# Performance work log

Hardware: AMD Instinct MI355X
Metric: run time of the kernel (lower is better)

## Reference

```python
import jax, jax.numpy as jnp
import numpy as np

B, C, E, H = 2, 2048, 1024, 16
HD = E // H


def setup_inputs() -> dict:
    key = jax.random.key(0)
    k_x, k_len, k_w1, k_b1, k_w2, k_b2 = jax.random.split(key, 6)
    x = jax.random.normal(k_x, (B, C, E), dtype=jnp.float32)
    # pad_mask: True where token is valid; random valid lengths in [C//2, C]
    lengths = jax.random.randint(k_len, (B,), C // 2, C + 1)
    pad_mask = jnp.arange(C)[None, :] < lengths[:, None]  # [B, C] bool
    s1 = 1.0 / np.sqrt(E)
    w_qkv = jax.random.uniform(k_w1, (3 * E, E), jnp.float32, -s1, s1)  # torch Linear weight [out,in]
    b_qkv = jax.random.uniform(k_b1, (3 * E,), jnp.float32, -s1, s1)
    w_out = jax.random.uniform(k_w2, (E, E), jnp.float32, -s1, s1)
    b_out = jax.random.uniform(k_b2, (E,), jnp.float32, -s1, s1)
    return {"x": x, "pad_mask": pad_mask, "w_qkv": w_qkv, "b_qkv": b_qkv,
            "w_out": w_out, "b_out": b_out}


def reference(x, pad_mask, w_qkv, b_qkv, w_out, b_out):
    b, c, e = x.shape
    qkv = x @ w_qkv.T + b_qkv                      # [B, C, 3E]
    qkv = qkv.reshape(b, c, 3, H, HD)
    qkv = jnp.transpose(qkv, (2, 0, 3, 1, 4))      # [3, B, H, C, HD]
    q, k, v = qkv[0], qkv[1], qkv[2]
    scores = jnp.einsum('bhqd,bhkd->bhqk', q, k) / np.sqrt(HD)  # [B,H,C,C]
    causal = jnp.tril(jnp.ones((c, c), dtype=bool))
    scores = jnp.where(causal[None, None, :, :], scores, -1e9)
    scores = jnp.where(pad_mask[:, None, None, :], scores, -1e9)
    attn = jax.nn.softmax(scores, axis=-1)
    out = jnp.einsum('bhqk,bhkd->bhqd', attn, v)   # [B,H,C,HD]
    out = jnp.transpose(out, (0, 2, 1, 3)).reshape(b, c, e)
    return out @ w_out.T + b_out
```

## Files before the change

### kernel.cpp

```cpp
#include <hip/hip_runtime.h>
#include <cstdint>
#include <cstddef>

typedef short short8 __attribute__((ext_vector_type(8)));
typedef float f32x4 __attribute__((ext_vector_type(4)));

#define NB 2
#define NC 2048
#define NE 1024
#define NH 16
#define ND 64
#define QSZ (NB*NH*NC*ND)

typedef const __attribute__((address_space(1))) void GV;
typedef __attribute__((address_space(3))) void LV;

__device__ __forceinline__ unsigned short f32_to_bf16(float f) {
    union { float f; unsigned u; } v; v.f = f;
    return (unsigned short)((v.u + 0x7fffu + ((v.u >> 16) & 1u)) >> 16);
}

__global__ __launch_bounds__(256) void fused_cast_kernel(
    const float* __restrict__ x, const float* __restrict__ wqkv,
    const float* __restrict__ wout, const void* __restrict__ pad,
    unsigned short* __restrict__ x_bf, unsigned short* __restrict__ wqkv_bf,
    unsigned short* __restrict__ wout_bf, int* __restrict__ lengths)
{
    const int bid = blockIdx.x, tid = threadIdx.x;
    if (bid < 8192) {
        const float* src; unsigned short* dst; int i;
        if (bid < 4096)      { src = x;    dst = x_bf;    i = bid*256 + tid; }
        else if (bid < 7168) { src = wqkv; dst = wqkv_bf; i = (bid-4096)*256 + tid; }
        else                 { src = wout; dst = wout_bf; i = (bid-7168)*256 + tid; }
        float4 v = ((const float4*)src)[i];
        ushort4 o;
        o.x = f32_to_bf16(v.x); o.y = f32_to_bf16(v.y);
        o.z = f32_to_bf16(v.z); o.w = f32_to_bf16(v.w);
        ((ushort4*)dst)[i] = o;
    } else {
        const int b = bid - 8192;
        unsigned w0 = ((const unsigned*)pad)[0];
        int cnt = 0;
        for (int i = tid; i < NC; i += 256) {
            int idx = b*NC + i;
            bool valid;
            if (w0 == 1u)               valid = ((const int*)pad)[idx] != 0;
            else if (w0 == 0x3f800000u) valid = ((const float*)pad)[idx] != 0.0f;
            else                        valid = ((const unsigned char*)pad)[idx] != 0;
            cnt += valid ? 1 : 0;
        }
        cnt += __shfl_xor(cnt, 1);  cnt += __shfl_xor(cnt, 2);
        cnt += __shfl_xor(cnt, 4);  cnt += __shfl_xor(cnt, 8);
        cnt += __shfl_xor(cnt, 16); cnt += __shfl_xor(cnt, 32);
        __shared__ int ws_[4];
        if ((tid & 63) == 0) ws_[tid >> 6] = cnt;
        __syncthreads();
        if (tid == 0) lengths[b] = ws_[0] + ws_[1] + ws_[2] + ws_[3];
    }
}

template<int EPI, int TM, int WPE>
__global__ __launch_bounds__(256, WPE) void gemm_bt_kernel(
    const unsigned short* __restrict__ A,
    const unsigned short* __restrict__ Bw,
    const float* __restrict__ bias,
    const int* __restrict__ lengths,
    float* __restrict__ outF,
    unsigned short* __restrict__ outQ,
    int M, int N, int K)
{
    constexpr int NF = (TM == 128) ? 4 : 2;
    constexpr int WCW = 16 * NF;
    __shared__ unsigned short As[TM*64];
    __shared__ unsigned short Bs[128*64];
    const int tid = threadIdx.x;
    const int w = tid >> 6, lane = tid & 63;
    const int wr = (TM == 128) ? (w >> 1) : 0;
    const int wc = (TM == 128) ? (w & 1) : w;
    const int g = lane >> 4, lr = lane & 15;
    const int nbx = N >> 7, nwg = gridDim.x;
    const int id = blockIdx.x;
    const int swz = (id & 7) * (nwg >> 3) + (id >> 3);
    const int mBase = (swz / nbx) * TM, nBase = (swz % nbx) * 128;

    if constexpr (EPI == 1) {
        if (nBase >= 1024) {
            const int lb = lengths[mBase >> 11];
            if ((mBase & 2047) >= ((lb + 63) & ~63)) return;
        }
    }

    f32x4 acc[4][NF];
#pragma unroll
    for (int m = 0; m < 4; ++m)
#pragma unroll
        for (int n = 0; n < NF; ++n) acc[m][n] = (f32x4){0.f, 0.f, 0.f, 0.f};

    constexpr int AJ = TM / 32;
    int srow[4], scol[4]; unsigned ldso[4];
#pragma unroll
    for (int j = 0; j < 4; ++j) {
        int o = ((j*4 + w) << 10) + lane*16;
        int row = o >> 7;
        int chunk = ((o >> 4) & 7) ^ (row & 7);
        srow[j] = row; scol[j] = chunk * 8; ldso[j] = (unsigned)((j*4 + w) << 10);
    }

    const int nk = K >> 6;
    for (int kt = 0; kt < nk; ++kt) {
        const int k0 = kt << 6;
#pragma unroll
        for (int j = 0; j < AJ; ++j) {
            const unsigned short* ga = A + (size_t)(mBase + srow[j])*K + (k0 + scol[j]);
            __builtin_amdgcn_global_load_lds((GV*)ga, (LV*)((char*)As + ldso[j]), 16, 0, 0);
        }
#pragma unroll
        for (int j = 0; j < 4; ++j) {
            const unsigned short* gb = Bw + (size_t)(nBase + srow[j])*K + (k0 + scol[j]);
            __builtin_amdgcn_global_load_lds((GV*)gb, (LV*)((char*)Bs + ldso[j]), 16, 0, 0);
        }
        __syncthreads();
#pragma unroll
        for (int ks = 0; ks < 2; ++ks) {
            short8 af[4], bf[NF];
#pragma unroll
            for (int m = 0; m < 4; ++m) {
                int row = wr*64 + m*16 + lr;
                int chunk = (ks*4 + g) ^ (row & 7);
                af[m] = *(const short8*)((const char*)As + row*128 + chunk*16);
            }
#pragma unroll
            for (int n = 0; n < NF; ++n) {
                int row = wc*WCW + n*16 + lr;
                int chunk = (ks*4 + g) ^ (row & 7);
                bf[n] = *(const short8*)((const char*)Bs + row*128 + chunk*16);
            }
#pragma unroll
            for (int m = 0; m < 4; ++m)
#pragma unroll
                for (int n = 0; n < NF; ++n)
                    acc[m][n] = __builtin_amdgcn_mfma_f32_16x16x32_bf16(af[m], bf[n], acc[m][n], 0, 0, 0);
        }
        __syncthreads();
    }

    if constexpr (EPI == 0) {
#pragma unroll
        for (int n = 0; n < NF; ++n) {
            int col = nBase + wc*WCW + n*16 + lr;
            float bv = bias[col];
#pragma unroll
            for (int m = 0; m < 4; ++m) {
                int rowb = mBase + wr*64 + m*16 + 4*g;
#pragma unroll
                for (int r = 0; r < 4; ++r)
                    outF[(size_t)(rowb + r)*N + col] = acc[m][n][r] + bv;
            }
        }
    } else {
        if (nBase >= 2048) {
#pragma unroll
            for (int n = 0; n < NF; ++n) {
                int col = nBase + wc*WCW + n*16 + lr;
                float bv = bias[col];
                int hh = (col >> 6) & 15, d = col & 63;
#pragma unroll
                for (int m = 0; m < 4; ++m) {
                    int rowb = mBase + wr*64 + m*16 + 4*g;
                    int bb = rowb >> 11, c = rowb & 2047;
                    int cp = (c & ~63) | ((m >> 1) << 5) | (g << 3) | ((m & 1) << 2);
                    size_t base = (((size_t)((4 + bb)*16 + hh))*64 + d)*2048 + cp;
                    float v0 = acc[m][n][0] + bv, v1 = acc[m][n][1] + bv;
                    float v2 = acc[m][n][2] + bv, v3 = acc[m][n][3] + bv;
                    unsigned w0, w1;
                    asm("v_cvt_pk_bf16_f32 %0, %1, %2" : "=v"(w0) : "v"(v0), "v"(v1));
                    asm("v_cvt_pk_bf16_f32 %0, %1, %2" : "=v"(w1) : "v"(v2), "v"(v3));
                    union { unsigned u[2]; uint2 v; } pk2; pk2.u[0] = w0; pk2.u[1] = w1;
                    *(uint2*)(outQ + base) = pk2.v;
                }
            }
        } else {
#pragma unroll
            for (int n = 0; n < NF; ++n) {
                int col = nBase + wc*WCW + n*16 + lr;
                float bv = bias[col];
                int t = col >> 10, hh = (col >> 6) & 15, d = col & 63;
                float qscale = (t == 0) ? 0.1803368801f : 1.0f;
#pragma unroll
                for (int m = 0; m < 4; ++m) {
                    int rowb = mBase + wr*64 + m*16 + 4*g;
#pragma unroll
                    for (int r = 0; r < 4; ++r) {
                        int row = rowb + r;
                        int bb = row >> 11, c = row & 2047;
                        unsigned short bf16v = f32_to_bf16((acc[m][n][r] + bv) * qscale);
                        size_t idx = ((((size_t)(t*2 + bb))*16 + hh)*2048 + c)*64 + d;
                        outQ[idx] = bf16v;
                    }
                }
            }
        }
    }
}

__global__ __launch_bounds__(256, 4) void attn_kernel(
    const unsigned short* __restrict__ qkv,
    const int* __restrict__ lengths,
    unsigned short* __restrict__ ctx)
{
    __shared__ unsigned short Kt[2][64*64];
    __shared__ unsigned short Vt[2][64*64];
    const int bh = blockIdx.x;
    const int b = bh >> 4, h = bh & 15;
    const int y = blockIdx.y;
    const int qb = (y < 8) ? 31 - y : (y < 16) ? y - 8 : (y < 24) ? 39 - y : y - 16;
    const int q0 = qb * 64;
    const int len = lengths[b];
    const int nt = min(qb + 1, (len + 63) >> 6);
    const int tid = threadIdx.x, w = tid >> 6, lane = tid & 63;
    const int g = lane >> 4, lr = lane & 15;
    const unsigned short* qp = qkv +          ((size_t)(b*NH + h))*NC*ND;
    const unsigned short* kp = qkv + QSZ    + ((size_t)(b*NH + h))*NC*ND;
    const unsigned short* vp = qkv + 2*QSZ  + ((size_t)(b*NH + h))*ND*NC;
    const int qw0 = q0 + w*16;

    short8 aq[2];
#pragma unroll
    for (int ks = 0; ks < 2; ++ks)
        aq[ks] = *(const short8*)(qp + (size_t)(qw0 + lr)*ND + ks*32 + 8*g);

    f32x4 oa[4];
#pragma unroll
    for (int n = 0; n < 4; ++n) oa[n] = (f32x4){0.f, 0.f, 0.f, 0.f};
    f32x4 acc_l = (f32x4){0.f, 0.f, 0.f, 0.f};
    union { unsigned u[4]; short8 s; } ones;
    ones.u[0] = ones.u[1] = ones.u[2] = ones.u[3] = 0x3F803F80u;

    int srw[2], sck[2]; unsigned ldso[2];
#pragma unroll
    for (int j = 0; j < 2; ++j) {
        int o = ((j*4 + w) << 10) + lane*16;
        int row = o >> 7;
        int chunk = ((o >> 4) & 7) ^ (row & 7);
        srw[j] = row; sck[j] = chunk * 8; ldso[j] = (unsigned)((j*4 + w) << 10);
    }

#define STAGE(T, BUF) do {                                                        \
    int k0s = (T) << 6;                                                           \
    _Pragma("unroll")                                                             \
    for (int j = 0; j < 2; ++j) {                                                 \
        const unsigned short* gk = kp + (size_t)(k0s + srw[j])*ND + sck[j];       \
        const unsigned short* gv = vp + (size_t)srw[j]*NC + k0s + sck[j];         \
        __builtin_amdgcn_global_load_lds((GV*)gk, (LV*)((char*)Kt[BUF] + ldso[j]), 16, 0, 0); \
        __builtin_amdgcn_global_load_lds((GV*)gv, (LV*)((char*)Vt[BUF] + ldso[j]), 16, 0, 0); \
    } } while (0)

    STAGE(0, 0);
    __syncthreads();

#pragma unroll 2
    for (int t = 0; t < nt; ++t) {
        if (t + 1 < nt) STAGE(t + 1, (t + 1) & 1);
        const char* Kb = (const char*)Kt[t & 1];
        const char* Vb = (const char*)Vt[t & 1];
        const int k0 = t << 6;

        f32x4 sa[4];
#pragma unroll
        for (int a = 0; a < 4; ++a) sa[a] = (f32x4){0.f, 0.f, 0.f, 0.f};
        __builtin_amdgcn_s_setprio(1);
#pragma unroll
        for (int ks = 0; ks < 2; ++ks) {
#pragma unroll
            for (int a = 0; a < 4; ++a) {
                int row = a*16 + lr;
                int chunk = (ks*4 + g) ^ (row & 7);
                short8 ak = *(const short8*)(Kb + row*128 + chunk*16);
                sa[a] = __builtin_amdgcn_mfma_f32_16x16x32_bf16(ak, aq[ks], sa[a], 0, 0, 0);
            }
        }
        __builtin_amdgcn_s_setprio(0);

        float p[4][4];
        const bool edge = (t == nt - 1);
        if (!edge) {
#pragma unroll
            for (int a = 0; a < 4; ++a)
#pragma unroll
                for (int r = 0; r < 4; ++r)
                    p[a][r] = exp2f(sa[a][r]);
        } else {
            const int qg = qw0 + lr;
            const int kb0 = k0 + 4*g;
#pragma unroll
            for (int a = 0; a < 4; ++a)
#pragma unroll
                for (int r = 0; r < 4; ++r) {
                    int key = kb0 + 16*a + r;
                    p[a][r] = (key <= qg && key < len) ? exp2f(sa[a][r]) : 0.f;
                }
        }

        unsigned pw0, pw1, pw2, pw3, pw4, pw5, pw6, pw7;
        asm("v_cvt_pk_bf16_f32 %0, %1, %2" : "=v"(pw0) : "v"(p[0][0]), "v"(p[0][1]));
        asm("v_cvt_pk_bf16_f32 %0, %1, %2" : "=v"(pw1) : "v"(p[0][2]), "v"(p[0][3]));
        asm("v_cvt_pk_bf16_f32 %0, %1, %2" : "=v"(pw2) : "v"(p[1][0]), "v"(p[1][1]));
        asm("v_cvt_pk_bf16_f32 %0, %1, %2" : "=v"(pw3) : "v"(p[1][2]), "v"(p[1][3]));
        asm("v_cvt_pk_bf16_f32 %0, %1, %2" : "=v"(pw4) : "v"(p[2][0]), "v"(p[2][1]));
        asm("v_cvt_pk_bf16_f32 %0, %1, %2" : "=v"(pw5) : "v"(p[2][2]), "v"(p[2][3]));
        asm("v_cvt_pk_bf16_f32 %0, %1, %2" : "=v"(pw6) : "v"(p[3][0]), "v"(p[3][1]));
        asm("v_cvt_pk_bf16_f32 %0, %1, %2" : "=v"(pw7) : "v"(p[3][2]), "v"(p[3][3]));
        union { unsigned u[4]; short8 s; } pu0, pu1;
        pu0.u[0] = pw0; pu0.u[1] = pw1; pu0.u[2] = pw2; pu0.u[3] = pw3;
        pu1.u[0] = pw4; pu1.u[1] = pw5; pu1.u[2] = pw6; pu1.u[3] = pw7;

        __builtin_amdgcn_s_setprio(1);
#pragma unroll
        for (int ks = 0; ks < 2; ++ks) {
            short8 pa = ks ? pu1.s : pu0.s;
            acc_l = __builtin_amdgcn_mfma_f32_16x16x32_bf16(pa, ones.s, acc_l, 0, 0, 0);
#pragma unroll
            for (int n = 0; n < 4; ++n) {
                int row = n*16 + lr;
                int chunk = (ks*4 + g) ^ (row & 7);
                short8 bv = *(const short8*)(Vb + row*128 + chunk*16);
                oa[n] = __builtin_amdgcn_mfma_f32_16x16x32_bf16(pa, bv, oa[n], 0, 0, 0);
            }
        }
        __builtin_amdgcn_s_setprio(0);

        __syncthreads();
    }
#undef STAGE

#pragma unroll
    for (int r = 0; r < 4; ++r) {
        float inv = 1.0f / acc_l[r];
        int qg = qw0 + 4*g + r;
        size_t base = ((size_t)b*NC + qg)*NE + h*ND;
#pragma unroll
        for (int n = 0; n < 4; ++n)
            ctx[base + n*16 + lr] = f32_to_bf16(oa[n][r] * inv);
    }
}

extern "C" void kernel_launch(void* const* d_in, const int* in_sizes, int n_in,
                              void* d_out, int out_size, void* d_ws, size_t ws_size,
                              hipStream_t stream)
{
    const float* x    = (const float*)d_in[0];
    const void*  pad  = d_in[1];
    const float* wqkv = (const float*)d_in[2];
    const float* bqkv = (const float*)d_in[3];
    const float* wout = (const float*)d_in[4];
    const float* bout = (const float*)d_in[5];
    float* out = (float*)d_out;

    unsigned short* x_bf    = (unsigned short*)d_ws;
    unsigned short* wqkv_bf = x_bf    + 4194304;
    unsigned short* wout_bf = wqkv_bf + 3145728;
    unsigned short* qkv     = wout_bf + 1048576;
    unsigned short* ctx     = qkv     + 12582912;
    int*            lens    = (int*)(ctx + 4194304);

    fused_cast_kernel<<<8194, 256, 0, stream>>>(x, wqkv, wout, pad,
                                                x_bf, wqkv_bf, wout_bf, lens);

    gemm_bt_kernel<1,128,3><<<768, 256, 0, stream>>>(x_bf, wqkv_bf, bqkv, lens,
                                                     nullptr, qkv, 4096, 3072, 1024);
    attn_kernel<<<dim3(32, 32), 256, 0, stream>>>(qkv, lens, ctx);
    gemm_bt_kernel<0,64,2><<<512, 256, 0, stream>>>(ctx, wout_bf, bout, nullptr,
                                                    out, nullptr, 4096, 1024, 1024);
}
```

Baseline: 90.90 us.

## Replace QKV GEMM with 256x256-tile, 8-wave pipelined kernel

Adds a dedicated QKV projection kernel that uses 256x256 output tiles with 512 threads, double-buffered direct-to-LDS loads with swizzling, and interleaved MFMA phases under s_setprio. The larger tiles raise arithmetic intensity, and the staged barrier schedule overlaps global loads with matrix math. It keeps the skip of K/V tiles past the padded length and writes the same Q/K/V/V-transposed layouts. The launch drops to 192 blocks, which may underfill the CUs on MI355X, and the high LDS and register use limits occupancy. The output GEMM now receives lens, which is probably unused in that epilogue.

```diff
diff --git a/kernel.cpp b/kernel.cpp
--- a/kernel.cpp
+++ b/kernel.cpp
@@ -59,6 +59,180 @@
     }
 }
 
+__global__ __launch_bounds__(512, 2) void gemm_qkv256_kernel(
+    const unsigned short* __restrict__ A,
+    const unsigned short* __restrict__ Bw,
+    const float* __restrict__ bias,
+    const int* __restrict__ lengths,
+    unsigned short* __restrict__ outQ)
+{
+    __shared__ unsigned short As[2*256*64];
+    __shared__ unsigned short Bs[2*256*64];
+    const int tid = threadIdx.x;
+    const int w = tid >> 6, lane = tid & 63;
+    const int wr = w >> 2, wc = w & 3;
+    const int g = lane >> 4, lr = lane & 15;
+    const int id = blockIdx.x;
+    const int swz = (id & 7) * 24 + (id >> 3);
+    const int mBase = (swz / 12) * 256, nBase = (swz % 12) * 256;
+
+    if (nBase >= 1024) {
+        const int lb = lengths[mBase >> 11];
+        if ((mBase & 2047) >= ((lb + 63) & ~63)) return;
+    }
+
+    f32x4 acc[8][4];
+#pragma unroll
+    for (int m = 0; m < 8; ++m)
+#pragma unroll
+        for (int n = 0; n < 4; ++n) acc[m][n] = (f32x4){0.f, 0.f, 0.f, 0.f};
+
+    const int srow = tid >> 3;
+    const int gcol = (((tid & 7) ^ ((tid >> 3) & 7)) << 3);
+    const unsigned ldw = (unsigned)(w << 10);
+
+#define STA(kt, h, buf) do { _Pragma("unroll")                                     \
+    for (int u = 0; u < 2; ++u) {                                                  \
+        const unsigned short* gp = A + (size_t)(mBase + (h)*128 + u*64 + srow)*1024 \
+                                     + ((kt) << 6) + gcol;                         \
+        __builtin_amdgcn_global_load_lds((GV*)gp,                                  \
+            (LV*)((char*)As + (buf)*32768 + (h)*16384 + u*8192 + ldw), 16, 0, 0);  \
+    } } while (0)
+#define STB(kt, h, buf) do { _Pragma("unroll")                                     \
+    for (int u = 0; u < 2; ++u) {                                                  \
+        const unsigned short* gp = Bw + (size_t)(nBase + (h)*128 + u*64 + srow)*1024 \
+                                     + ((kt) << 6) + gcol;                         \
+        __builtin_amdgcn_global_load_lds((GV*)gp,                                  \
+            (LV*)((char*)Bs + (buf)*32768 + (h)*16384 + u*8192 + ldw), 16, 0, 0);  \
+    } } while (0)
+#define RDA(buf, mh) do { _Pragma("unroll")                                        \
+    for (int mf = 0; mf < 4; ++mf) { _Pragma("unroll")                             \
+    for (int kk = 0; kk < 2; ++kk) {                                               \
+        int row = wr*128 + (mh)*64 + mf*16 + lr;                                   \
+        int chunk = (kk*4 + g) ^ (row & 7);                                        \
+        af[mf][kk] = *(const short8*)((const char*)As + (buf)*32768 + row*128 + chunk*16); \
+    } } } while (0)
+#define RDB(buf, nh, BG) do { _Pragma("unroll")                                    \
+    for (int nf = 0; nf < 2; ++nf) { _Pragma("unroll")                             \
+    for (int kk = 0; kk < 2; ++kk) {                                               \
+        int row = wc*64 + (nh)*32 + nf*16 + lr;                                    \
+        int chunk = (kk*4 + g) ^ (row & 7);                                        \
+        BG[nf][kk] = *(const short8*)((const char*)Bs + (buf)*32768 + row*128 + chunk*16); \
+    } } } while (0)
+#define MMQ(mh, nh, BG) do { _Pragma("unroll")                                     \
+    for (int mf = 0; mf < 4; ++mf) { _Pragma("unroll")                             \
+    for (int nf = 0; nf < 2; ++nf) { _Pragma("unroll")                             \
+    for (int kk = 0; kk < 2; ++kk)                                                 \
+        acc[(mh)*4+mf][(nh)*2+nf] = __builtin_amdgcn_mfma_f32_16x16x32_bf16(       \
+            af[mf][kk], BG[nf][kk], acc[(mh)*4+mf][(nh)*2+nf], 0, 0, 0);           \
+    } } } while (0)
+#define BAR __builtin_amdgcn_s_barrier()
+#define PRIO1 __builtin_amdgcn_s_setprio(1)
+#define PRIO0 __builtin_amdgcn_s_setprio(0)
+
+    short8 af[4][2], bg0[2][2], bg1[2][2];
+
+    STB(0, 0, 0); STB(0, 1, 0); STA(0, 0, 0); STA(0, 1, 0);
+    STB(1, 0, 1); STB(1, 1, 1); STA(1, 0, 1);
+    asm volatile("s_waitcnt vmcnt(6)" ::: "memory");
+    BAR;
+
+    for (int kt = 0; kt < 14; ++kt) {
+        const int b = kt & 1, b1 = b ^ 1;
+        RDA(b, 0); RDB(b, 0, bg0);
+        STA(kt + 1, 1, b1);
+        BAR;
+        PRIO1; MMQ(0, 0, bg0); PRIO0;
+        BAR;
+        RDB(b, 1, bg1);
+        BAR;
+        PRIO1; MMQ(0, 1, bg1); PRIO0;
+        BAR;
+        RDA(b, 1);
+        STB(kt + 2, 0, b);
+        BAR;
+        PRIO1; MMQ(1, 0, bg0); PRIO0;
+        BAR;
+        STB(kt + 2, 1, b); STA(kt + 2, 0, b);
+        asm volatile("s_waitcnt vmcnt(6)" ::: "memory");
+        BAR;
+        PRIO1; MMQ(1, 1, bg1); PRIO0;
+        BAR;
+    }
+    {
+        RDA(0, 0); RDB(0, 0, bg0);
+        STA(15, 1, 1);
+        BAR; PRIO1; MMQ(0, 0, bg0); PRIO0; BAR;
+        RDB(0, 1, bg1);
+        BAR; PRIO1; MMQ(0, 1, bg1); PRIO0; BAR;
+        RDA(0, 1);
+        BAR; PRIO1; MMQ(1, 0, bg0); PRIO0; BAR;
+        asm volatile("s_waitcnt vmcnt(0)" ::: "memory");
+        BAR;
+        PRIO1; MMQ(1, 1, bg1); PRIO0;
+        BAR;
+    }
+    {
+        RDA(1, 0); RDB(1, 0, bg0); MMQ(0, 0, bg0);
+        RDB(1, 1, bg1); MMQ(0, 1, bg1);
+        RDA(1, 1); MMQ(1, 0, bg0); MMQ(1, 1, bg1);
+    }
+
+#undef STA
+#undef STB
+#undef RDA
+#undef RDB
+#undef MMQ
+#undef BAR
+#undef PRIO1
+#undef PRIO0
+
+    if (nBase >= 2048) {
+#pragma unroll
+        for (int n = 0; n < 4; ++n) {
+            const int col = nBase + wc*64 + n*16 + lr;
+            const float bv = bias[col];
+            const int hh = (col >> 6) & 15, d = col & 63;
+#pragma unroll
+            for (int m = 0; m < 8; ++m) {
+                int rowb = mBase + wr*128 + m*16 + 4*g;
+                int bb = rowb >> 11, c = rowb & 2047;
+                int mq = m & 3;
+                int cp = (c & ~63) | ((mq >> 1) << 5) | (g << 3) | ((mq & 1) << 2);
+                size_t base = (((size_t)((4 + bb)*16 + hh))*64 + d)*2048 + cp;
+                float v0 = acc[m][n][0] + bv, v1 = acc[m][n][1] + bv;
+                float v2 = acc[m][n][2] + bv, v3 = acc[m][n][3] + bv;
+                unsigned w0, w1;
+                asm("v_cvt_pk_bf16_f32 %0, %1, %2" : "=v"(w0) : "v"(v0), "v"(v1));
+                asm("v_cvt_pk_bf16_f32 %0, %1, %2" : "=v"(w1) : "v"(v2), "v"(v3));
+                union { unsigned u[2]; uint2 v; } pk2; pk2.u[0] = w0; pk2.u[1] = w1;
+                *(uint2*)(outQ + base) = pk2.v;
+            }
+        }
+    } else {
+        const int t = nBase >> 10;
+        const float qscale = (t == 0) ? 0.1803368801f : 1.0f;
+#pragma unroll
+        for (int n = 0; n < 4; ++n) {
+            const int col = nBase + wc*64 + n*16 + lr;
+            const float bv = bias[col];
+            const int hh = (col >> 6) & 15, d = col & 63;
+#pragma unroll
+            for (int m = 0; m < 8; ++m) {
+                int rowb = mBase + wr*128 + m*16 + 4*g;
+#pragma unroll
+                for (int r = 0; r < 4; ++r) {
+                    int row = rowb + r;
+                    int bb = row >> 11, c = row & 2047;
+                    unsigned short bf16v = f32_to_bf16((acc[m][n][r] + bv) * qscale);
+                    size_t idx = ((((size_t)(t*2 + bb))*16 + hh)*2048 + c)*64 + d;
+                    outQ[idx] = bf16v;
+                }
+            }
+        }
+    }
+}
+
 template<int EPI, int TM, int WPE>
 __global__ __launch_bounds__(256, WPE) void gemm_bt_kernel(
     const unsigned short* __restrict__ A,
@@ -366,9 +540,8 @@
     fused_cast_kernel<<<8194, 256, 0, stream>>>(x, wqkv, wout, pad,
                                                 x_bf, wqkv_bf, wout_bf, lens);
 
-    gemm_bt_kernel<1,128,3><<<768, 256, 0, stream>>>(x_bf, wqkv_bf, bqkv, lens,
-                                                     nullptr, qkv, 4096, 3072, 1024);
+    gemm_qkv256_kernel<<<192, 512, 0, stream>>>(x_bf, wqkv_bf, bqkv, lens, qkv);
     attn_kernel<<<dim3(32, 32), 256, 0, stream>>>(qkv, lens, ctx);
-    gemm_bt_kernel<0,64,2><<<512, 256, 0, stream>>>(ctx, wout_bf, bout, nullptr,
+    gemm_bt_kernel<0,64,2><<<512, 256, 0, stream>>>(ctx, wout_bf, bout, lens,
                                                     out, nullptr, 4096, 1024, 1024);
 }
```

Measured after the change: 99.48 us. 1.09x slower.

## Widen attention blocks to 128 query rows with 512 threads sharing K/V tiles

Applied to the files above, without the earlier changes.

The attention kernel now uses 512-thread blocks covering 128 query rows (8 waves), so each staged 64-key K/V tile is reused by twice as many queries and the grid halves. Each thread issues one global-to-LDS load per tile instead of two. The causal/padding mask test becomes a per-wave check, because waves in the top half of a block see tiles that are fully unmasked for them. The output GEMM now also receives the lengths pointer, possibly so it can skip padded rows. The cost is coarser causal load balancing, since the upper-half waves do redundant masked work on the last tile, plus a higher per-block register and occupancy demand.

```diff
diff --git a/kernel.cpp b/kernel.cpp
--- a/kernel.cpp
+++ b/kernel.cpp
@@ -203,7 +203,7 @@
     }
 }
 
-__global__ __launch_bounds__(256, 4) void attn_kernel(
+__global__ __launch_bounds__(512, 4) void attn_kernel(
     const unsigned short* __restrict__ qkv,
     const int* __restrict__ lengths,
     unsigned short* __restrict__ ctx)
@@ -213,16 +213,17 @@
     const int bh = blockIdx.x;
     const int b = bh >> 4, h = bh & 15;
     const int y = blockIdx.y;
-    const int qb = (y < 8) ? 31 - y : (y < 16) ? y - 8 : (y < 24) ? 39 - y : y - 16;
-    const int q0 = qb * 64;
+    const int u = (y < 8) ? 15 - y : y - 8;
+    const int q0 = u * 128;
     const int len = lengths[b];
-    const int nt = min(qb + 1, (len + 63) >> 6);
+    const int lenceil = (len + 63) >> 6;
+    const int nt = min(2*u + 2, lenceil);
     const int tid = threadIdx.x, w = tid >> 6, lane = tid & 63;
     const int g = lane >> 4, lr = lane & 15;
     const unsigned short* qp = qkv +          ((size_t)(b*NH + h))*NC*ND;
     const unsigned short* kp = qkv + QSZ    + ((size_t)(b*NH + h))*NC*ND;
     const unsigned short* vp = qkv + 2*QSZ  + ((size_t)(b*NH + h))*ND*NC;
-    const int qw0 = q0 + w*16;
+    const int qw0 = q0 + (w >> 2)*64 + (w & 3)*16;
 
     short8 aq[2];
 #pragma unroll
@@ -236,24 +237,21 @@
     union { unsigned u[4]; short8 s; } ones;
     ones.u[0] = ones.u[1] = ones.u[2] = ones.u[3] = 0x3F803F80u;
 
-    int srw[2], sck[2]; unsigned ldso[2];
-#pragma unroll
-    for (int j = 0; j < 2; ++j) {
-        int o = ((j*4 + w) << 10) + lane*16;
+    int srw_, sck_; unsigned ldso_;
+    {
+        int o = (w << 10) + lane*16;
         int row = o >> 7;
         int chunk = ((o >> 4) & 7) ^ (row & 7);
-        srw[j] = row; sck[j] = chunk * 8; ldso[j] = (unsigned)((j*4 + w) << 10);
+        srw_ = row; sck_ = chunk * 8; ldso_ = (unsigned)(w << 10);
     }
 
 #define STAGE(T, BUF) do {                                                        \
     int k0s = (T) << 6;                                                           \
-    _Pragma("unroll")                                                             \
-    for (int j = 0; j < 2; ++j) {                                                 \
-        const unsigned short* gk = kp + (size_t)(k0s + srw[j])*ND + sck[j];       \
-        const unsigned short* gv = vp + (size_t)srw[j]*NC + k0s + sck[j];         \
-        __builtin_amdgcn_global_load_lds((GV*)gk, (LV*)((char*)Kt[BUF] + ldso[j]), 16, 0, 0); \
-        __builtin_amdgcn_global_load_lds((GV*)gv, (LV*)((char*)Vt[BUF] + ldso[j]), 16, 0, 0); \
-    } } while (0)
+    const unsigned short* gk = kp + (size_t)(k0s + srw_)*ND + sck_;               \
+    const unsigned short* gv = vp + (size_t)srw_*NC + k0s + sck_;                 \
+    __builtin_amdgcn_global_load_lds((GV*)gk, (LV*)((char*)Kt[BUF] + ldso_), 16, 0, 0); \
+    __builtin_amdgcn_global_load_lds((GV*)gv, (LV*)((char*)Vt[BUF] + ldso_), 16, 0, 0); \
+    } while (0)
 
     STAGE(0, 0);
     __syncthreads();
@@ -282,8 +280,8 @@
         __builtin_amdgcn_s_setprio(0);
 
         float p[4][4];
-        const bool edge = (t == nt - 1);
-        if (!edge) {
+        const bool fast = ((k0 + 63) <= qw0) && (k0 + 64 <= len);
+        if (fast) {
 #pragma unroll
             for (int a = 0; a < 4; ++a)
 #pragma unroll
@@ -368,7 +366,7 @@
 
     gemm_bt_kernel<1,128,3><<<768, 256, 0, stream>>>(x_bf, wqkv_bf, bqkv, lens,
                                                      nullptr, qkv, 4096, 3072, 1024);
-    attn_kernel<<<dim3(32, 32), 256, 0, stream>>>(qkv, lens, ctx);
-    gemm_bt_kernel<0,64,2><<<512, 256, 0, stream>>>(ctx, wout_bf, bout, nullptr,
+    attn_kernel<<<dim3(32, 16), 512, 0, stream>>>(qkv, lens, ctx);
+    gemm_bt_kernel<0,64,2><<<512, 256, 0, stream>>>(ctx, wout_bf, bout, lens,
                                                     out, nullptr, 4096, 1024, 1024);
 }
```

Measured after the change: 95.57 us. 5.1% more time.
